# Performance work log

Hardware: AMD Instinct MI355X
Metric: run time of the kernel (lower is better)

Reference implementation:

```python
import jax, jax.numpy as jnp
import numpy as np

ALPHA = 0.2  # LeakyReLU negative slope
EDGE_NUM = 3


def _gat(q_nodes, v, adj, a_q, a_v):
    # q_nodes: (b,n,d_hidden), v: (b,n,d_model), adj: (b,n,n)
    # e_ij = LeakyReLU(a_q . h_i + a_v . v_j)  (decomposition of a^T[h_i;v_j])
    s_q = jnp.einsum('bnd,d->bn', q_nodes, a_q)
    s_v = jnp.einsum('bne,e->bn', v, a_v)
    e = jax.nn.leaky_relu(s_q[:, :, None] + s_v[:, None, :], negative_slope=ALPHA)
    e = jnp.where(adj > 0, e, -1e9)
    attn = jax.nn.softmax(e, axis=-1)           # (b,n,n)
    return jnp.einsum('bij,bje->bie', attn, v)  # (b,n,d_model)


def setup_inputs() -> dict:
    key = jax.random.key(0)
    ks = jax.random.split(key, 16)
    b, n, dh, dm = 8, 1024, 512, 512
    s = 0.02
    inp = {
        'nodes': jax.random.normal(ks[0], (b, n, dh), dtype=jnp.float32),
        'mask': jax.random.randint(ks[1], (2, b, n, n), 0, 2, dtype=jnp.int32),
        'node_type': jax.random.randint(ks[2], (b, n), 0, 5, dtype=jnp.int64),
        # edge-typed linears (bias=False), stacked over 3 edge types
        'W_in': jax.random.normal(ks[3], (EDGE_NUM, dh, dm), dtype=jnp.float32) * s,
        'W_out': jax.random.normal(ks[4], (EDGE_NUM, dh, dm), dtype=jnp.float32) * s,
        # GAT attention vectors, split into query / value halves
        'a_in_q': jax.random.normal(ks[5], (dh,), dtype=jnp.float32) * s,
        'a_in_v': jax.random.normal(ks[6], (dm,), dtype=jnp.float32) * s,
        'a_out_q': jax.random.normal(ks[7], (dh,), dtype=jnp.float32) * s,
        'a_out_v': jax.random.normal(ks[8], (dm,), dtype=jnp.float32) * s,
        # GGNN propagator (reset / update / transform)
        'W_r': jax.random.normal(ks[9], (3 * dm, dm), dtype=jnp.float32) * s,
        'b_r': jnp.zeros((dm,), dtype=jnp.float32),
        'W_z': jax.random.normal(ks[10], (3 * dm, dm), dtype=jnp.float32) * s,
        'b_z': jnp.zeros((dm,), dtype=jnp.float32),
        'W_t': jax.random.normal(ks[11], (3 * dm, dm), dtype=jnp.float32) * s,
        'b_t': jnp.zeros((dm,), dtype=jnp.float32),
    }
    return inp


def reference(nodes, mask, node_type, W_in, W_out, a_in_q, a_in_v, a_out_q, a_out_v,
              W_r, b_r, W_z, b_z, W_t, b_t):
    # type masks for tags 2,3,4 -> (3,b,n)
    tags = jnp.arange(2, 2 + EDGE_NUM, dtype=node_type.dtype)
    tmask = (node_type[None, :, :] == tags[:, None, None]).astype(nodes.dtype)
    # edge-typed linear + masked sum over edge types
    node_in = jnp.sum(jnp.einsum('bnd,tde->tbne', nodes, W_in) * tmask[..., None], axis=0)
    node_out = jnp.sum(jnp.einsum('bnd,tde->tbne', nodes, W_out) * tmask[..., None], axis=0)
    # GAT-style masked attention (in / out edges); dropout = identity (eval)
    h_in = _gat(nodes, node_in, mask[0], a_in_q, a_in_v)
    h_out = _gat(nodes, node_out, mask[1], a_out_q, a_out_v)
    # GGNN gated propagator
    a = jnp.concatenate([h_in, h_out, nodes], axis=-1)
    r = jax.nn.sigmoid(a @ W_r + b_r)
    z = jax.nn.sigmoid(a @ W_z + b_z)
    joint = jnp.concatenate([h_in, h_out, r * nodes], axis=-1)
    h_hat = jnp.tanh(joint @ W_t + b_t)
    return (1.0 - z) * nodes + z * h_hat
```

## Files before the change

### kernel.cpp

```cpp
#include <hip/hip_runtime.h>
#include <hip/hip_bf16.h>
#include <stdint.h>

typedef unsigned short u16;
typedef __attribute__((ext_vector_type(8))) short bf16x8;
typedef __attribute__((ext_vector_type(4))) float floatx4;

__device__ __forceinline__ float bf2f(u16 v){ return __uint_as_float(((unsigned)v)<<16); }
__device__ __forceinline__ u16 f2bf(float f){
  unsigned u = __float_as_uint(f);
  unsigned r = 0x7fffu + ((u>>16)&1u);
  return (u16)((u+r)>>16);
}
__device__ __forceinline__ float lrelu(float x){ return x > 0.f ? x : 0.2f*x; }
__device__ __forceinline__ float sigm(float t){
  t = fminf(fmaxf(t, -30.f), 30.f);
  return 1.f/(1.f + expf(-t));
}

#define GLOAD16(ldsdst, gsrc) \
  __builtin_amdgcn_global_load_lds((const __attribute__((address_space(1))) void*)(gsrc), \
      (__attribute__((address_space(3))) void*)(ldsdst), 16, 0, 0)

__global__ void k_detect(const u16* __restrict__ nodes_raw,
                         const int* __restrict__ ntype_raw, int* flags)
{
  __shared__ int s_wild, s_nz;
  if (threadIdx.x == 0){ s_wild = 0; s_nz = 0; }
  __syncthreads();
  int wild = 0;
#pragma unroll
  for (int i = 0; i < 16; i++){
    u16 w = nodes_raw[threadIdx.x*16 + i];
    int e = (w >> 7) & 0xFF;
    if (e != 0 && (e < 102 || e > 152)) wild++;
  }
  int nz = 0;
  if (threadIdx.x < 255 && ntype_raw[2*threadIdx.x + 1] != 0) nz = 1;
  atomicAdd(&s_wild, wild);
  atomicAdd(&s_nz, nz);
  __syncthreads();
  if (threadIdx.x == 0){
    flags[0] = (s_wild > 1024) ? 1 : 0;
    flags[1] = (s_nz == 0) ? 1 : 0;
  }
}

struct CanonDesc {
  const void* src[13];
  u16*        dst[13];
  int startBlk[13];
  int n4[13];
};
__global__ __launch_bounds__(256)
void k_canon_all(CanonDesc d, u16* __restrict__ X, const int* __restrict__ flags)
{
  int blk = blockIdx.x;
  int seg = 0;
#pragma unroll
  for (int s = 1; s < 13; s++) if (blk >= d.startBlk[s]) seg = s;
  int i = (blk - d.startBlk[seg])*256 + threadIdx.x;
  if (i >= d.n4[seg]) return;
  uint2 bits;
  if (flags[0]) {
    float4 v = ((const float4*)d.src[seg])[i];
    ushort4 o2;
    o2.x = f2bf(v.x); o2.y = f2bf(v.y); o2.z = f2bf(v.z); o2.w = f2bf(v.w);
    bits = *(uint2*)&o2;
  } else {
    bits = ((const uint2*)d.src[seg])[i];
  }
  ((uint2*)d.dst[seg])[i] = bits;
  if (seg == 0) {
    int e0 = i*4;
    long r = e0 >> 9;
    int  c = e0 & 511;
    *(uint2*)&X[r*2048 + c] = bits;
  }
}

__global__ void k_build_idx(const int* __restrict__ ntype, const int* __restrict__ flags,
                            int* __restrict__ idx, int* __restrict__ cnt)
{
  __shared__ int c[3];
  if (threadIdx.x < 3) c[threadIdx.x] = 0;
  __syncthreads();
  const int i64 = flags[1];
  for (int i = threadIdx.x; i < 8192; i += 256){
    int t = i64 ? ntype[2*i] : ntype[i];
    if (t >= 2 && t <= 4){
      int p = atomicAdd(&c[t-2], 1);
      idx[(t-2)*8192 + p] = i;
    }
  }
  __syncthreads();
  if (threadIdx.x < 3) cnt[threadIdx.x] = c[threadIdx.x];
}

template<int MODE, class Epi>
__global__ __launch_bounds__(256)
void gemm_bt(const u16* __restrict__ A, int ldA, long sAz,
             const u16* __restrict__ B, int ldB, long sBz,
             int K, Epi epi)
{
  __shared__ __align__(16) u16 As[2][128][32];
  __shared__ __align__(16) u16 Bs[2][128][32];
  int bm, bn, bz;
  if (MODE == 0){ bm = blockIdx.x; bn = blockIdx.y; bz = blockIdx.z; }
  else          { bz = blockIdx.x; bn = blockIdx.y; bm = blockIdx.z; }
  const int tid  = threadIdx.x;
  const int lane = tid & 63;
  const int wave = tid >> 6;
  const int wm = (wave & 1) << 6;
  const int wn = (wave >> 1) << 6;
  const int mrow = lane & 15;
  const int quad = lane >> 4;

  const u16* Ab = A + (long)bz*sAz + (long)bm*128*ldA;
  const u16* Bb = B + (long)bz*sBz + (long)bn*128*ldB;
  const int srow = tid >> 2;
  const int scol = (tid & 3) << 3;
  const u16* gA0 = Ab + (long)srow*ldA + scol;
  const u16* gA1 = Ab + (long)(srow+64)*ldA + scol;
  const u16* gB0 = Bb + (long)srow*ldB + scol;
  const u16* gB1 = Bb + (long)(srow+64)*ldB + scol;

  floatx4 acc[4][4];
#pragma unroll
  for (int i=0;i<4;i++)
#pragma unroll
    for (int j=0;j<4;j++) acc[i][j] = 0.f;

  auto issue = [&](int buf){
    GLOAD16(&As[buf][srow][scol],    gA0);
    GLOAD16(&As[buf][srow+64][scol], gA1);
    GLOAD16(&Bs[buf][srow][scol],    gB0);
    GLOAD16(&Bs[buf][srow+64][scol], gB1);
    gA0 += 32; gA1 += 32; gB0 += 32; gB1 += 32;
  };

  issue(0);
  const int nIter = K >> 5;
  for (int it = 0; it < nIter; ++it) {
    const int cur = it & 1;
    asm volatile("s_waitcnt vmcnt(0)" ::: "memory");
    __syncthreads();
    if (it + 1 < nIter) issue(cur ^ 1);
    bf16x8 af[4], bfr[4];
#pragma unroll
    for (int i=0;i<4;i++) af[i]  = *(const bf16x8*)&As[cur][wm + i*16 + mrow][quad*8];
#pragma unroll
    for (int i=0;i<4;i++) bfr[i] = *(const bf16x8*)&Bs[cur][wn + i*16 + mrow][quad*8];
#pragma unroll
    for (int mi=0;mi<4;mi++)
#pragma unroll
      for (int ni=0;ni<4;ni++)
        acc[mi][ni] = __builtin_amdgcn_mfma_f32_16x16x32_bf16(af[mi], bfr[ni], acc[mi][ni], 0,0,0);
  }

#pragma unroll
  for (int mi=0;mi<4;mi++)
#pragma unroll
    for (int ni=0;ni<4;ni++) {
      const int col  = (bn<<7) + wn + ni*16 + mrow;
      const int row0 = (bm<<7) + wm + mi*16 + quad*4;
#pragma unroll
      for (int r=0;r<4;r++)
        epi(row0 + r, col, bz, acc[mi][ni][r]);
    }
}

__global__ __launch_bounds__(256)
void gemm_typed(const u16* __restrict__ A, const u16* __restrict__ B,
                const int* __restrict__ idx, const int* __restrict__ cnt,
                u16* __restrict__ node_in, u16* __restrict__ node_out)
{
  const int bz = blockIdx.z;
  const int count = cnt[bz];
  const int m0 = blockIdx.x << 7;
  if (m0 >= count) return;
  __shared__ __align__(16) u16 As[2][128][32];
  __shared__ __align__(16) u16 Bs[2][128][32];
  const int bn = blockIdx.y;
  const int tid  = threadIdx.x;
  const int lane = tid & 63;
  const int wave = tid >> 6;
  const int wm = (wave & 1) << 6;
  const int wn = (wave >> 1) << 6;
  const int mrow = lane & 15;
  const int quad = lane >> 4;
  const int* myidx = idx + bz*8192;

  const int srow = tid >> 2;
  const int scol = (tid & 3) << 3;
  int r0i = m0 + srow;      if (r0i >= count) r0i = m0;
  int r1i = m0 + srow + 64; if (r1i >= count) r1i = m0;
  const u16* gA0 = A + (long)myidx[r0i]*512 + scol;
  const u16* gA1 = A + (long)myidx[r1i]*512 + scol;
  const u16* Bb = B + (long)bz*1024*512 + (long)bn*128*512;
  const u16* gB0 = Bb + (long)srow*512 + scol;
  const u16* gB1 = Bb + (long)(srow+64)*512 + scol;

  floatx4 acc[4][4];
#pragma unroll
  for (int i=0;i<4;i++)
#pragma unroll
    for (int j=0;j<4;j++) acc[i][j] = 0.f;

  auto issue = [&](int buf){
    GLOAD16(&As[buf][srow][scol],    gA0);
    GLOAD16(&As[buf][srow+64][scol], gA1);
    GLOAD16(&Bs[buf][srow][scol],    gB0);
    GLOAD16(&Bs[buf][srow+64][scol], gB1);
    gA0 += 32; gA1 += 32; gB0 += 32; gB1 += 32;
  };

  issue(0);
  for (int it = 0; it < 16; ++it) {
    const int cur = it & 1;
    asm volatile("s_waitcnt vmcnt(0)" ::: "memory");
    __syncthreads();
    if (it + 1 < 16) issue(cur ^ 1);
    bf16x8 af[4], bfr[4];
#pragma unroll
    for (int i=0;i<4;i++) af[i]  = *(const bf16x8*)&As[cur][wm + i*16 + mrow][quad*8];
#pragma unroll
    for (int i=0;i<4;i++) bfr[i] = *(const bf16x8*)&Bs[cur][wn + i*16 + mrow][quad*8];
#pragma unroll
    for (int mi=0;mi<4;mi++)
#pragma unroll
      for (int ni=0;ni<4;ni++)
        acc[mi][ni] = __builtin_amdgcn_mfma_f32_16x16x32_bf16(af[mi], bfr[ni], acc[mi][ni], 0,0,0);
  }

#pragma unroll
  for (int mi=0;mi<4;mi++) {
    const int lr0 = wm + mi*16 + quad*4;
#pragma unroll
    for (int r=0;r<4;r++) {
      const int lr = lr0 + r;
      if (m0 + lr >= count) continue;
      const long orig = myidx[m0 + lr];
#pragma unroll
      for (int ni=0;ni<4;ni++) {
        const int col = (bn<<7) + wn + ni*16 + mrow;
        u16 h = f2bf(acc[mi][ni][r]);
        if (col < 512) node_in [orig*512 + col]       = h;
        else           node_out[orig*512 + (col-512)] = h;
      }
    }
  }
}

struct EpiPV {
  const float* inv_l; u16* X; int colOff;
  __device__ void operator()(int row, int col, int bz, float v) const {
    long gr = (long)bz*1024 + row;
    X[gr*2048 + colOff + col] = f2bf(v * inv_l[gr]);
  }
};
struct EpiG1 {
  const u16* nodes; const u16* b_r; const u16* b_z; u16* X; u16* zbuf;
  __device__ void operator()(int row, int col, int bz, float v) const {
    if (col < 512) {
      float r = sigm(v + bf2f(b_r[col]));
      X[(long)row*2048 + 1536 + col] = f2bf(r * bf2f(nodes[(long)row*512 + col]));
    } else {
      int c = col - 512;
      zbuf[(long)row*512 + c] = f2bf(sigm(v + bf2f(b_z[c])));
    }
  }
};
struct EpiG2 {
  const u16* zbuf; const u16* nodes; const u16* b_t; const int* flags; void* out;
  __device__ void operator()(int row, int col, int bz, float v) const {
    long idx = (long)row*512 + col;
    float t = fminf(fmaxf(v + bf2f(b_t[col]), -15.f), 15.f);
    float h = tanhf(t);
    float z = bf2f(zbuf[idx]);
    float nv = bf2f(nodes[idx]);
    float o2 = (1.f - z)*nv + z*h;
    if (flags[0]) ((float*)out)[idx] = o2;
    else          ((u16*)out)[idx]   = f2bf(o2);
  }
};

struct TrDesc {
  const u16* src[9]; u16* dst[9]; int rot[9]; int ldD[9]; int rows[9]; int modK[9];
};
__global__ __launch_bounds__(256)
void k_wtrans(TrDesc d)
{
  __shared__ u16 tile[32][33];
  const int z = blockIdx.z;
  const int r0 = blockIdx.y*32;
  if (r0 >= d.rows[z]) return;
  const u16* src = d.src[z];
  u16* dst = d.dst[z];
  const int c0 = blockIdx.x*32;
  const int tx = threadIdx.x, ty = threadIdx.y;
#pragma unroll
  for (int i=0;i<32;i+=8)
    tile[ty+i][tx] = src[(long)(r0+ty+i)*512 + c0 + tx];
  __syncthreads();
  const int k0 = (r0 + d.rot[z]) % d.modK[z];
#pragma unroll
  for (int i=0;i<32;i+=8)
    dst[(long)(c0+ty+i)*d.ldD[z] + k0 + tx] = tile[tx][ty+i];
}

__global__ __launch_bounds__(256)
void k_vtrans(const u16* __restrict__ nin, const u16* __restrict__ nout,
              u16* __restrict__ vin, u16* __restrict__ vout)
{
  __shared__ u16 tile[32][33];
  const int z = blockIdx.z;
  const int b = z & 7;
  const u16* src = (z < 8 ? nin : nout) + (long)b*1024*512;
  u16* dst = (z < 8 ? vin : vout) + (long)b*512*1024;
  const int c0 = blockIdx.x*32, r0 = blockIdx.y*32;
  const int tx = threadIdx.x, ty = threadIdx.y;
#pragma unroll
  for (int i=0;i<32;i+=8)
    tile[ty+i][tx] = src[(long)(r0+ty+i)*512 + c0 + tx];
  __syncthreads();
#pragma unroll
  for (int i=0;i<32;i+=8)
    dst[(long)(c0+ty+i)*1024 + r0 + tx] = tile[tx][ty+i];
}

__device__ __forceinline__ void load8f(float* f, const u16* p){
  uint4 q = *(const uint4*)p;
  unsigned w[4] = {q.x, q.y, q.z, q.w};
#pragma unroll
  for (int i=0;i<4;i++){ f[2*i] = bf2f((u16)(w[i]&0xffffu)); f[2*i+1] = bf2f((u16)(w[i]>>16)); }
}

__global__ __launch_bounds__(256)
void k_svec(const u16* __restrict__ nodes, const u16* __restrict__ nin, const u16* __restrict__ nout,
            const u16* __restrict__ aiq, const u16* __restrict__ aiv,
            const u16* __restrict__ aoq, const u16* __restrict__ aov,
            float* sq_in, float* sq_out, float* sv_in, float* sv_out)
{
  const int lane = threadIdx.x & 63, wave = threadIdx.x >> 6;
  const long row = (long)blockIdx.x*4 + wave;
  const int c = lane << 3;
  float xn[8], xi[8], xo[8], q1[8], v1[8], q2[8], v2[8];
  load8f(xn, nodes + row*512 + c);
  load8f(xi, nin   + row*512 + c);
  load8f(xo, nout  + row*512 + c);
  load8f(q1, aiq + c); load8f(v1, aiv + c);
  load8f(q2, aoq + c); load8f(v2, aov + c);
  float s0=0,s1=0,s2=0,s3=0;
#pragma unroll
  for (int j=0;j<8;j++){ s0 += xn[j]*q1[j]; s1 += xn[j]*q2[j]; s2 += xi[j]*v1[j]; s3 += xo[j]*v2[j]; }
#pragma unroll
  for (int off=32; off; off>>=1){
    s0 += __shfl_xor(s0, off);
    s1 += __shfl_xor(s1, off);
    s2 += __shfl_xor(s2, off);
    s3 += __shfl_xor(s3, off);
  }
  if (lane==0){ sq_in[row]=s0; sq_out[row]=s1; sv_in[row]=s2; sv_out[row]=s3; }
}

__global__ __launch_bounds__(256)
void k_stats(const int* __restrict__ mask, const float* __restrict__ sq,
             const float* __restrict__ sv, u16* __restrict__ P, float* __restrict__ inv_l)
{
  const int lane = threadIdx.x & 63, wave = threadIdx.x >> 6;
  const long row = (long)blockIdx.x*4 + wave;
  const long b = row >> 10;
  const int* mrow = mask + row*1024;
  const float* svb = sv + b*1024;
  const float qs = sq[row];
  float m = -3.0e38f;
  float e[4][4];
#pragma unroll
  for (int it=0; it<4; ++it) {
    int j = it*256 + lane*4;
    int4 mk = *(const int4*)&mrow[j];
    float4 s = *(const float4*)&svb[j];
    e[it][0] = mk.x > 0 ? lrelu(qs + s.x) : -1e9f;
    e[it][1] = mk.y > 0 ? lrelu(qs + s.y) : -1e9f;
    e[it][2] = mk.z > 0 ? lrelu(qs + s.z) : -1e9f;
    e[it][3] = mk.w > 0 ? lrelu(qs + s.w) : -1e9f;
    m = fmaxf(m, fmaxf(fmaxf(e[it][0], e[it][1]), fmaxf(e[it][2], e[it][3])));
  }
#pragma unroll
  for (int off=32; off; off>>=1) m = fmaxf(m, __shfl_xor(m, off));
  float l = 0.f;
#pragma unroll
  for (int it=0; it<4; ++it) {
    int j = it*256 + lane*4;
    float p0 = expf(e[it][0] - m), p1 = expf(e[it][1] - m);
    float p2 = expf(e[it][2] - m), p3 = expf(e[it][3] - m);
    ushort4 pk;
    pk.x = f2bf(p0); pk.y = f2bf(p1); pk.z = f2bf(p2); pk.w = f2bf(p3);
    *(ushort4*)&P[row*1024 + j] = pk;
    l += (p0 + p1) + (p2 + p3);
  }
#pragma unroll
  for (int off=32; off; off>>=1) l += __shfl_xor(l, off);
  if (lane==0) inv_l[row] = 1.f / l;
}

extern "C" void kernel_launch(void* const* d_in, const int* in_sizes, int n_in,
                              void* d_out, int out_size, void* d_ws, size_t ws_size,
                              hipStream_t stream)
{
  const void* nodes_r   = d_in[0];
  const int*  mask      = (const int*)d_in[1];
  const int*  ntype     = (const int*)d_in[2];

  char* base = (char*)d_ws;
  size_t o = 0;
  auto alloc = [&](size_t bytes){ void* p = base + o; o += (bytes + 255) & ~size_t(255); return p; };
  int*  flags   = (int*)alloc(256);
  int*  cnt     = (int*)alloc(256);
  int*  idx     = (int*)alloc(3ll*8192*4);
  u16* cn_nodes = (u16*)alloc(8192ll*512*2);
  u16* cn_Win   = (u16*)alloc(3ll*512*512*2);
  u16* cn_Wout  = (u16*)alloc(3ll*512*512*2);
  u16* cn_Wr    = (u16*)alloc(1536ll*512*2);
  u16* cn_Wz    = (u16*)alloc(1536ll*512*2);
  u16* cn_Wt    = (u16*)alloc(1536ll*512*2);
  u16* cn_aiq   = (u16*)alloc(512*2);
  u16* cn_aiv   = (u16*)alloc(512*2);
  u16* cn_aoq   = (u16*)alloc(512*2);
  u16* cn_aov   = (u16*)alloc(512*2);
  u16* cn_br    = (u16*)alloc(512*2);
  u16* cn_bz    = (u16*)alloc(512*2);
  u16* cn_bt    = (u16*)alloc(512*2);
  u16* node_in  = (u16*)alloc(8192ll*512*2);
  u16* node_out = (u16*)alloc(8192ll*512*2);
  u16* VtIn     = (u16*)alloc(8ll*512*1024*2);
  u16* VtOut    = (u16*)alloc(8ll*512*1024*2);
  u16* X        = (u16*)alloc(8192ll*2048*2);
  u16* P        = (u16*)alloc(8ll*1024*1024*2);
  u16* Wio_t    = (u16*)alloc(3ll*1024*512*2);
  u16* Wrz_t    = (u16*)alloc(1024ll*1536*2);
  u16* Wt_t     = (u16*)alloc(512ll*1536*2);
  float* sq_in  = (float*)alloc(8192*4);
  float* sq_out = (float*)alloc(8192*4);
  float* sv_in  = (float*)alloc(8192*4);
  float* sv_out = (float*)alloc(8192*4);
  float* il_in  = (float*)alloc(8192*4);
  float* il_out = (float*)alloc(8192*4);
  u16* zbuf = node_in;

  hipMemsetAsync(node_in, 0, 2ll*8192*512*2, stream);

  k_detect<<<1, 256, 0, stream>>>((const u16*)nodes_r, ntype, flags);

  CanonDesc cd;
  const int canonN[13] = {8192*512, 3*512*512, 3*512*512, 1536*512, 1536*512, 1536*512,
                          512,512,512,512,512,512,512};
  u16* canonDst[13] = {cn_nodes, cn_Win, cn_Wout, cn_Wr, cn_Wz, cn_Wt,
                       cn_aiq, cn_aiv, cn_aoq, cn_aov, cn_br, cn_bz, cn_bt};
  const int canonSrcIdx[13] = {0,3,4,9,11,13,5,6,7,8,10,12,14};
  int blk = 0;
  for (int s=0;s<13;s++){
    cd.src[s] = d_in[canonSrcIdx[s]];
    cd.dst[s] = canonDst[s];
    cd.n4[s]  = canonN[s]/4;
    cd.startBlk[s] = blk;
    blk += (cd.n4[s] + 255)/256;
  }
  k_canon_all<<<blk, 256, 0, stream>>>(cd, X, flags);

  k_build_idx<<<1, 256, 0, stream>>>(ntype, flags, idx, cnt);

  TrDesc td;
  td.src[0]=cn_Wr; td.src[1]=cn_Wz; td.src[2]=cn_Wt;
  td.dst[0]=Wrz_t; td.dst[1]=Wrz_t + 512ll*1536; td.dst[2]=Wt_t;
  td.rot[0]=512; td.rot[1]=512; td.rot[2]=0;
  td.ldD[0]=1536; td.ldD[1]=1536; td.ldD[2]=1536;
  td.rows[0]=1536; td.rows[1]=1536; td.rows[2]=1536;
  td.modK[0]=1536; td.modK[1]=1536; td.modK[2]=1536;
  for (int t=0;t<3;t++){
    td.src[3+t]=cn_Win  + (long)t*512*512; td.dst[3+t]=Wio_t + (long)t*1024*512;
    td.src[6+t]=cn_Wout + (long)t*512*512; td.dst[6+t]=Wio_t + (long)t*1024*512 + 512ll*512;
    td.rot[3+t]=td.rot[6+t]=0; td.ldD[3+t]=td.ldD[6+t]=512;
    td.rows[3+t]=td.rows[6+t]=512; td.modK[3+t]=td.modK[6+t]=512;
  }
  k_wtrans<<<dim3(16,48,9), dim3(32,8), 0, stream>>>(td);

  gemm_typed<<<dim3(64,8,3), 256, 0, stream>>>(cn_nodes, Wio_t, idx, cnt, node_in, node_out);

  k_vtrans<<<dim3(16,32,16), dim3(32,8), 0, stream>>>(node_in, node_out, VtIn, VtOut);

  k_svec<<<2048, 256, 0, stream>>>(cn_nodes, node_in, node_out, cn_aiq, cn_aiv, cn_aoq, cn_aov,
                                   sq_in, sq_out, sv_in, sv_out);

  k_stats<<<2048, 256, 0, stream>>>(mask, sq_in, sv_in, P, il_in);
  gemm_bt<1><<<dim3(8,4,8), 256, 0, stream>>>(P, 1024, 1024ll*1024, VtIn, 1024, 512ll*1024, 1024,
                                              EpiPV{il_in, X, 512});
  k_stats<<<2048, 256, 0, stream>>>(mask + 8ll*1024*1024, sq_out, sv_out, P, il_out);
  gemm_bt<1><<<dim3(8,4,8), 256, 0, stream>>>(P, 1024, 1024ll*1024, VtOut, 1024, 512ll*1024, 1024,
                                              EpiPV{il_out, X, 1024});

  gemm_bt<0><<<dim3(64,8,1), 256, 0, stream>>>(X, 2048, 0ll, Wrz_t, 1536, 0ll, 1536,
                                               EpiG1{cn_nodes, cn_br, cn_bz, X, zbuf});
  gemm_bt<0><<<dim3(64,4,1), 256, 0, stream>>>(X + 512, 2048, 0ll, Wt_t, 1536, 0ll, 1536,
                                               EpiG2{zbuf, cn_nodes, cn_bt, flags, (void*)d_out});
}
```

Before: 397.4 us.

## Deepen GEMM LDS pipeline to 4 stages and batch in/out attention launches

Both GEMM kernels move from a double-buffered LDS pipeline to four buffers with three tiles in flight. They use partial vmcnt waits and a raw s_barrier so global loads overlap MFMA work for longer. The two k_stats and two P·V GEMM launches are merged into single launches over 16 batch slices, with P, Vt and the score arrays sized to match, which fills more CUs per launch. expf and tanhf are replaced with __expf and a sigmoid-based tanh to make the transcendentals cheaper. The cost is double the LDS per block (lower occupancy), a larger P buffer, and slightly lower precision in the fast exponentials.

```diff
diff --git a/kernel.cpp b/kernel.cpp
--- a/kernel.cpp
+++ b/kernel.cpp
@@ -15,7 +15,7 @@
 __device__ __forceinline__ float lrelu(float x){ return x > 0.f ? x : 0.2f*x; }
 __device__ __forceinline__ float sigm(float t){
   t = fminf(fmaxf(t, -30.f), 30.f);
-  return 1.f/(1.f + expf(-t));
+  return 1.f/(1.f + __expf(-t));
 }
 
 #define GLOAD16(ldsdst, gsrc) \
@@ -103,8 +103,8 @@
              const u16* __restrict__ B, int ldB, long sBz,
              int K, Epi epi)
 {
-  __shared__ __align__(16) u16 As[2][128][32];
-  __shared__ __align__(16) u16 Bs[2][128][32];
+  __shared__ __align__(16) u16 As[4][128][32];
+  __shared__ __align__(16) u16 Bs[4][128][32];
   int bm, bn, bz;
   if (MODE == 0){ bm = blockIdx.x; bn = blockIdx.y; bz = blockIdx.z; }
   else          { bz = blockIdx.x; bn = blockIdx.y; bm = blockIdx.z; }
@@ -139,13 +139,16 @@
     gA0 += 32; gA1 += 32; gB0 += 32; gB1 += 32;
   };
 
-  issue(0);
+  issue(0); issue(1); issue(2);
   const int nIter = K >> 5;
   for (int it = 0; it < nIter; ++it) {
-    const int cur = it & 1;
-    asm volatile("s_waitcnt vmcnt(0)" ::: "memory");
-    __syncthreads();
-    if (it + 1 < nIter) issue(cur ^ 1);
+    const int cur = it & 3;
+    const int rem = nIter - 1 - it;
+    if (rem >= 2)      asm volatile("s_waitcnt vmcnt(8)" ::: "memory");
+    else if (rem == 1) asm volatile("s_waitcnt vmcnt(4)" ::: "memory");
+    else               asm volatile("s_waitcnt vmcnt(0)" ::: "memory");
+    asm volatile("s_barrier" ::: "memory");
+    if (it + 3 < nIter) issue((it + 3) & 3);
     bf16x8 af[4], bfr[4];
 #pragma unroll
     for (int i=0;i<4;i++) af[i]  = *(const bf16x8*)&As[cur][wm + i*16 + mrow][quad*8];
@@ -179,8 +182,8 @@
   const int count = cnt[bz];
   const int m0 = blockIdx.x << 7;
   if (m0 >= count) return;
-  __shared__ __align__(16) u16 As[2][128][32];
-  __shared__ __align__(16) u16 Bs[2][128][32];
+  __shared__ __align__(16) u16 As[4][128][32];
+  __shared__ __align__(16) u16 Bs[4][128][32];
   const int bn = blockIdx.y;
   const int tid  = threadIdx.x;
   const int lane = tid & 63;
@@ -215,12 +218,15 @@
     gA0 += 32; gA1 += 32; gB0 += 32; gB1 += 32;
   };
 
-  issue(0);
+  issue(0); issue(1); issue(2);
   for (int it = 0; it < 16; ++it) {
-    const int cur = it & 1;
-    asm volatile("s_waitcnt vmcnt(0)" ::: "memory");
-    __syncthreads();
-    if (it + 1 < 16) issue(cur ^ 1);
+    const int cur = it & 3;
+    const int rem = 15 - it;
+    if (rem >= 2)      asm volatile("s_waitcnt vmcnt(8)" ::: "memory");
+    else if (rem == 1) asm volatile("s_waitcnt vmcnt(4)" ::: "memory");
+    else               asm volatile("s_waitcnt vmcnt(0)" ::: "memory");
+    asm volatile("s_barrier" ::: "memory");
+    if (it + 3 < 16) issue((it + 3) & 3);
     bf16x8 af[4], bfr[4];
 #pragma unroll
     for (int i=0;i<4;i++) af[i]  = *(const bf16x8*)&As[cur][wm + i*16 + mrow][quad*8];
@@ -253,10 +259,11 @@
 }
 
 struct EpiPV {
-  const float* inv_l; u16* X; int colOff;
+  const float* il; u16* X;
   __device__ void operator()(int row, int col, int bz, float v) const {
-    long gr = (long)bz*1024 + row;
-    X[gr*2048 + colOff + col] = f2bf(v * inv_l[gr]);
+    long gr = (long)(bz & 7)*1024 + row;
+    int colOff = 512 + ((bz >> 3) << 9);
+    X[gr*2048 + colOff + col] = f2bf(v * il[(long)(bz>>3)*8192 + gr]);
   }
 };
 struct EpiG1 {
@@ -276,7 +283,7 @@
   __device__ void operator()(int row, int col, int bz, float v) const {
     long idx = (long)row*512 + col;
     float t = fminf(fmaxf(v + bf2f(b_t[col]), -15.f), 15.f);
-    float h = tanhf(t);
+    float h = 2.f*sigm(2.f*t) - 1.f;
     float z = bf2f(zbuf[idx]);
     float nv = bf2f(nodes[idx]);
     float o2 = (1.f - z)*nv + z*h;
@@ -340,7 +347,7 @@
 void k_svec(const u16* __restrict__ nodes, const u16* __restrict__ nin, const u16* __restrict__ nout,
             const u16* __restrict__ aiq, const u16* __restrict__ aiv,
             const u16* __restrict__ aoq, const u16* __restrict__ aov,
-            float* sq_in, float* sq_out, float* sv_in, float* sv_out)
+            float* sq_all, float* sv_all)
 {
   const int lane = threadIdx.x & 63, wave = threadIdx.x >> 6;
   const long row = (long)blockIdx.x*4 + wave;
@@ -361,19 +368,22 @@
     s2 += __shfl_xor(s2, off);
     s3 += __shfl_xor(s3, off);
   }
-  if (lane==0){ sq_in[row]=s0; sq_out[row]=s1; sv_in[row]=s2; sv_out[row]=s3; }
-}
-
-__global__ __launch_bounds__(256)
-void k_stats(const int* __restrict__ mask, const float* __restrict__ sq,
-             const float* __restrict__ sv, u16* __restrict__ P, float* __restrict__ inv_l)
+  if (lane==0){
+    sq_all[row] = s0; sq_all[8192 + row] = s1;
+    sv_all[row] = s2; sv_all[8192 + row] = s3;
+  }
+}
+
+__global__ __launch_bounds__(256)
+void k_stats(const int* __restrict__ mask, const float* __restrict__ sq_all,
+             const float* __restrict__ sv_all, u16* __restrict__ P, float* __restrict__ il_all)
 {
   const int lane = threadIdx.x & 63, wave = threadIdx.x >> 6;
   const long row = (long)blockIdx.x*4 + wave;
-  const long b = row >> 10;
-  const int* mrow = mask + row*1024;
-  const float* svb = sv + b*1024;
-  const float qs = sq[row];
+  const long gr  = (long)blockIdx.y*8192 + row;
+  const int* mrow = mask + gr*1024;
+  const float* svb = sv_all + (long)blockIdx.y*8192 + (row >> 10)*1024;
+  const float qs = sq_all[gr];
   float m = -3.0e38f;
   float e[4][4];
 #pragma unroll
@@ -393,25 +403,25 @@
 #pragma unroll
   for (int it=0; it<4; ++it) {
     int j = it*256 + lane*4;
-    float p0 = expf(e[it][0] - m), p1 = expf(e[it][1] - m);
-    float p2 = expf(e[it][2] - m), p3 = expf(e[it][3] - m);
+    float p0 = __expf(e[it][0] - m), p1 = __expf(e[it][1] - m);
+    float p2 = __expf(e[it][2] - m), p3 = __expf(e[it][3] - m);
     ushort4 pk;
     pk.x = f2bf(p0); pk.y = f2bf(p1); pk.z = f2bf(p2); pk.w = f2bf(p3);
-    *(ushort4*)&P[row*1024 + j] = pk;
+    *(ushort4*)&P[gr*1024 + j] = pk;
     l += (p0 + p1) + (p2 + p3);
   }
 #pragma unroll
   for (int off=32; off; off>>=1) l += __shfl_xor(l, off);
-  if (lane==0) inv_l[row] = 1.f / l;
+  if (lane==0) il_all[gr] = 1.f / l;
 }
 
 extern "C" void kernel_launch(void* const* d_in, const int* in_sizes, int n_in,
                               void* d_out, int out_size, void* d_ws, size_t ws_size,
                               hipStream_t stream)
 {
-  const void* nodes_r   = d_in[0];
-  const int*  mask      = (const int*)d_in[1];
-  const int*  ntype     = (const int*)d_in[2];
+  const void* nodes_r = d_in[0];
+  const int*  mask    = (const int*)d_in[1];
+  const int*  ntype   = (const int*)d_in[2];
 
   char* base = (char*)d_ws;
   size_t o = 0;
@@ -434,19 +444,15 @@
   u16* cn_bt    = (u16*)alloc(512*2);
   u16* node_in  = (u16*)alloc(8192ll*512*2);
   u16* node_out = (u16*)alloc(8192ll*512*2);
-  u16* VtIn     = (u16*)alloc(8ll*512*1024*2);
-  u16* VtOut    = (u16*)alloc(8ll*512*1024*2);
+  u16* Vt       = (u16*)alloc(16ll*512*1024*2);
   u16* X        = (u16*)alloc(8192ll*2048*2);
-  u16* P        = (u16*)alloc(8ll*1024*1024*2);
+  u16* P        = (u16*)alloc(16ll*1024*1024*2);
   u16* Wio_t    = (u16*)alloc(3ll*1024*512*2);
   u16* Wrz_t    = (u16*)alloc(1024ll*1536*2);
   u16* Wt_t     = (u16*)alloc(512ll*1536*2);
-  float* sq_in  = (float*)alloc(8192*4);
-  float* sq_out = (float*)alloc(8192*4);
-  float* sv_in  = (float*)alloc(8192*4);
-  float* sv_out = (float*)alloc(8192*4);
-  float* il_in  = (float*)alloc(8192*4);
-  float* il_out = (float*)alloc(8192*4);
+  float* sq_all = (float*)alloc(16384*4);
+  float* sv_all = (float*)alloc(16384*4);
+  float* il_all = (float*)alloc(16384*4);
   u16* zbuf = node_in;
 
   hipMemsetAsync(node_in, 0, 2ll*8192*512*2, stream);
@@ -488,17 +494,15 @@
 
   gemm_typed<<<dim3(64,8,3), 256, 0, stream>>>(cn_nodes, Wio_t, idx, cnt, node_in, node_out);
 
-  k_vtrans<<<dim3(16,32,16), dim3(32,8), 0, stream>>>(node_in, node_out, VtIn, VtOut);
+  k_vtrans<<<dim3(16,32,16), dim3(32,8), 0, stream>>>(node_in, node_out, Vt, Vt + 8ll*512*1024);
 
   k_svec<<<2048, 256, 0, stream>>>(cn_nodes, node_in, node_out, cn_aiq, cn_aiv, cn_aoq, cn_aov,
-                                   sq_in, sq_out, sv_in, sv_out);
-
-  k_stats<<<2048, 256, 0, stream>>>(mask, sq_in, sv_in, P, il_in);
-  gemm_bt<1><<<dim3(8,4,8), 256, 0, stream>>>(P, 1024, 1024ll*1024, VtIn, 1024, 512ll*1024, 1024,
-                                              EpiPV{il_in, X, 512});
-  k_stats<<<2048, 256, 0, stream>>>(mask + 8ll*1024*1024, sq_out, sv_out, P, il_out);
-  gemm_bt<1><<<dim3(8,4,8), 256, 0, stream>>>(P, 1024, 1024ll*1024, VtOut, 1024, 512ll*1024, 1024,
-                                              EpiPV{il_out, X, 1024});
+                                   sq_all, sv_all);
+
+  k_stats<<<dim3(2048,2), 256, 0, stream>>>(mask, sq_all, sv_all, P, il_all);
+
+  gemm_bt<1><<<dim3(16,4,8), 256, 0, stream>>>(P, 1024, 1024ll*1024, Vt, 1024, 512ll*1024, 1024,
+                                               EpiPV{il_all, X});
 
   gemm_bt<0><<<dim3(64,8,1), 256, 0, stream>>>(X, 2048, 0ll, Wrz_t, 1536, 0ll, 1536,
                                                EpiG1{cn_nodes, cn_br, cn_bz, X, zbuf});
```

Result: faster. 375.0 us (-5.6%).
